# Optimization experiments

Hardware: AMD Instinct MI355X
Metric: run time of the kernel (lower is better)

Reference implementation:

```python
import jax, jax.numpy as jnp
import numpy as np

Z_DIM = 128
K = 64
RANK = 16
B = 65536


def setup_inputs() -> dict:
    key = jax.random.key(0)
    k1, k2, k3 = jax.random.split(key, 3)
    z = jax.random.normal(k1, (B, Z_DIM), dtype=jnp.float32)
    # nn.Linear(z_dim, K*rank): weight [K*rank, z_dim], bias [K*rank]
    bound = 1.0 / np.sqrt(Z_DIM)
    W = jax.random.uniform(k2, (K * RANK, Z_DIM), dtype=jnp.float32, minval=-bound, maxval=bound)
    b = jax.random.uniform(k3, (K * RANK,), dtype=jnp.float32, minval=-bound, maxval=bound)
    return {"z": z, "W": W, "b": b}


def reference(z, W, b):
    bsz = z.shape[0]
    # linear projection: [B, K*rank]
    w = z @ W.T + b
    w = w.reshape(bsz, K, RANK) + 1e-6
    # batched reduced QR on small K x rank matrices (fp32, like torch .float())
    q, _ = jnp.linalg.qr(w.astype(jnp.float32), mode="reduced")
    return q.astype(z.dtype)
```

## Files before the change

kernel.cpp:

```cpp
#include <hip/hip_runtime.h>

#define TOTAL_B 65536
#define NKR 1024
#define ZD 128

__global__ __launch_bounds__(256) void gemm_zwt(
    const float* __restrict__ z, const float* __restrict__ W,
    const float* __restrict__ bias, float* __restrict__ out)
{
    __shared__ float zs[32][132];
    __shared__ float ws[32][132];

    const int tid = threadIdx.x;
    const int tx = tid & 15;
    const int ty = tid >> 4;
    const int m0 = blockIdx.y * 128;
    const int n0 = blockIdx.x * 128;

    float acc[8][8];
    #pragma unroll
    for (int i = 0; i < 8; ++i)
        #pragma unroll
        for (int j = 0; j < 8; ++j) acc[i][j] = 0.f;

    const int kq = (tid & 7) * 4;
    const int mr = tid >> 3;

    const float* gz = z + (size_t)(m0 + mr) * ZD + kq;
    const float* gw = W + (size_t)(n0 + mr) * ZD + kq;

    float4 vz[4], vw[4];
    #pragma unroll
    for (int p = 0; p < 4; ++p) {
        vz[p] = *(const float4*)(gz + (size_t)p * 32 * ZD);
        vw[p] = *(const float4*)(gw + (size_t)p * 32 * ZD);
    }

    #pragma unroll
    for (int kc = 0; kc < ZD; kc += 32) {
        #pragma unroll
        for (int p = 0; p < 4; ++p) {
            int ml = mr + p * 32;
            zs[kq + 0][ml] = vz[p].x; zs[kq + 1][ml] = vz[p].y;
            zs[kq + 2][ml] = vz[p].z; zs[kq + 3][ml] = vz[p].w;
            ws[kq + 0][ml] = vw[p].x; ws[kq + 1][ml] = vw[p].y;
            ws[kq + 2][ml] = vw[p].z; ws[kq + 3][ml] = vw[p].w;
        }
        __syncthreads();

        if (kc + 32 < ZD) {
            #pragma unroll
            for (int p = 0; p < 4; ++p) {
                vz[p] = *(const float4*)(gz + (size_t)p * 32 * ZD + kc + 32);
                vw[p] = *(const float4*)(gw + (size_t)p * 32 * ZD + kc + 32);
            }
        }

        #pragma unroll 8
        for (int k = 0; k < 32; ++k) {
            float4 a0 = *(const float4*)&zs[k][ty * 4];
            float4 a1 = *(const float4*)&zs[k][64 + ty * 4];
            float4 c0 = *(const float4*)&ws[k][tx * 4];
            float4 c1 = *(const float4*)&ws[k][64 + tx * 4];
            float zr[8] = {a0.x, a0.y, a0.z, a0.w, a1.x, a1.y, a1.z, a1.w};
            float wr[8] = {c0.x, c0.y, c0.z, c0.w, c1.x, c1.y, c1.z, c1.w};
            #pragma unroll
            for (int i = 0; i < 8; ++i)
                #pragma unroll
                for (int j = 0; j < 8; ++j)
                    acc[i][j] = fmaf(zr[i], wr[j], acc[i][j]);
        }
        __syncthreads();
    }

    float bv0[4], bv1[4];
    #pragma unroll
    for (int j = 0; j < 4; ++j) {
        bv0[j] = bias[n0 + tx * 4 + j] + 1e-6f;
        bv1[j] = bias[n0 + 64 + tx * 4 + j] + 1e-6f;
    }

    #pragma unroll
    for (int i = 0; i < 8; ++i) {
        int row = (i < 4) ? (ty * 4 + i) : (64 + ty * 4 + i - 4);
        size_t base = (size_t)(m0 + row) * NKR + n0;
        float4 o0, o1;
        o0.x = acc[i][0] + bv0[0]; o0.y = acc[i][1] + bv0[1];
        o0.z = acc[i][2] + bv0[2]; o0.w = acc[i][3] + bv0[3];
        o1.x = acc[i][4] + bv1[0]; o1.y = acc[i][5] + bv1[1];
        o1.z = acc[i][6] + bv1[2]; o1.w = acc[i][7] + bv1[3];
        *(float4*)(out + base + tx * 4) = o0;
        *(float4*)(out + base + 64 + tx * 4) = o1;
    }
}

template <int CTRL>
__device__ __forceinline__ float dpp_add(float v) {
    int x = __builtin_amdgcn_update_dpp(0, __float_as_int(v), CTRL, 0xF, 0xF, false);
    return v + __int_as_float(x);
}

__device__ __forceinline__ float rsum16(float v) {
    v = dpp_add<0x128>(v);
    v = dpp_add<0x124>(v);
    v = dpp_add<0x122>(v);
    v = dpp_add<0x121>(v);
    return v;
}

__global__ __launch_bounds__(256) void qr_batched(float* __restrict__ buf)
{
    const int tid = threadIdx.x;
    const int lq = tid & 15;
    const int item = (blockIdx.x * 256 + tid) >> 4;

    float* p = buf + (size_t)item * NKR + lq * 16;

    float a[16][4];
    #pragma unroll
    for (int i = 0; i < 4; ++i) {
        #pragma unroll
        for (int cc = 0; cc < 16; cc += 4) {
            float4 v = *(const float4*)(p + i * 256 + cc);
            a[cc + 0][i] = v.x; a[cc + 1][i] = v.y;
            a[cc + 2][i] = v.z; a[cc + 3][i] = v.w;
        }
    }

    float tau[16];

    #pragma unroll
    for (int j = 0; j < 16; ++j) {
        float x0 = a[j][0], x1 = a[j][1], x2 = a[j][2], x3 = a[j][3];
        float x0m = (lq > j) ? x0 : 0.f;
        float pp = fmaf(x0m, x0m, fmaf(x1, x1, fmaf(x2, x2, x3 * x3)));
        float xn2   = rsum16(pp);
        float alpha = rsum16((lq == j) ? x0 : 0.f);

        float rr   = __builtin_amdgcn_sqrtf(fmaf(alpha, alpha, xn2));
        float beta = (alpha >= 0.f) ? -rr : rr;
        float dba  = beta - alpha;
        float tj   = dba * __builtin_amdgcn_rcpf(beta);
        float sc   = -__builtin_amdgcn_rcpf(dba);
        if (xn2 == 0.f) { tj = 0.f; sc = 0.f; }
        tau[j] = tj;

        float v0 = (lq == j) ? 1.f : ((lq > j) ? x0 * sc : 0.f);
        float v1 = x1 * sc, v2 = x2 * sc, v3 = x3 * sc;
        a[j][0] = v0; a[j][1] = v1; a[j][2] = v2; a[j][3] = v3;

        #pragma unroll
        for (int c = j + 1; c < 16; ++c) {
            float d = rsum16(fmaf(v0, a[c][0],
                        fmaf(v1, a[c][1],
                        fmaf(v2, a[c][2], v3 * a[c][3]))));
            float t = -tj * d;
            a[c][0] = fmaf(t, v0, a[c][0]);
            a[c][1] = fmaf(t, v1, a[c][1]);
            a[c][2] = fmaf(t, v2, a[c][2]);
            a[c][3] = fmaf(t, v3, a[c][3]);
        }
    }

    #pragma unroll
    for (int j = 15; j >= 0; --j) {
        float tj = tau[j];
        float v0 = a[j][0], v1 = a[j][1], v2 = a[j][2], v3 = a[j][3];
        #pragma unroll
        for (int c = j + 1; c < 16; ++c) {
            float d = rsum16(fmaf(v0, a[c][0],
                        fmaf(v1, a[c][1],
                        fmaf(v2, a[c][2], v3 * a[c][3]))));
            float t = -tj * d;
            a[c][0] = fmaf(t, v0, a[c][0]);
            a[c][1] = fmaf(t, v1, a[c][1]);
            a[c][2] = fmaf(t, v2, a[c][2]);
            a[c][3] = fmaf(t, v3, a[c][3]);
        }
        float nt = -tj;
        a[j][0] = fmaf(nt, v0, (lq == j) ? 1.f : 0.f);
        a[j][1] = nt * v1;
        a[j][2] = nt * v2;
        a[j][3] = nt * v3;
    }

    #pragma unroll
    for (int i = 0; i < 4; ++i) {
        #pragma unroll
        for (int cc = 0; cc < 16; cc += 4) {
            float4 vv = {a[cc + 0][i], a[cc + 1][i], a[cc + 2][i], a[cc + 3][i]};
            *(float4*)(p + i * 256 + cc) = vv;
        }
    }
}

extern "C" void kernel_launch(void* const* d_in, const int* in_sizes, int n_in,
                              void* d_out, int out_size, void* d_ws, size_t ws_size,
                              hipStream_t stream) {
    const float* z = (const float*)d_in[0];
    const float* W = (const float*)d_in[1];
    const float* b = (const float*)d_in[2];
    float* out = (float*)d_out;

    dim3 ggrid(NKR / 128, TOTAL_B / 128);
    hipLaunchKernelGGL(gemm_zwt, ggrid, dim3(256), 0, stream, z, W, b, out);
    hipLaunchKernelGGL(qr_batched, dim3(TOTAL_B / 16), dim3(256), 0, stream, out);
}
```

Measured before the change: 605.1 us.

## Store GEMM tiles row-major in LDS and use strided thread-to-output mapping

The GEMM kernel now keeps z and W tiles in shared memory in their natural row-major layout, padded to 36, instead of transposing them on store. The inner loop reads float4 along K and does four FMAs per pair. The thread-to-output mapping becomes strided (ty+16i, tx+16j), so outputs are written as scalar stores, coalesced across threads, instead of float4 stores. The grid is swapped so blockIdx.x walks the batch dimension, and the register prefetch of the next K chunk is dropped, which removes overlap between global loads and compute.

Result: slower. 625.5 us (+3.4%).

```diff
diff --git a/kernel.cpp b/kernel.cpp
--- a/kernel.cpp
+++ b/kernel.cpp
@@ -8,14 +8,14 @@
     const float* __restrict__ z, const float* __restrict__ W,
     const float* __restrict__ bias, float* __restrict__ out)
 {
-    __shared__ float zs[32][132];
-    __shared__ float ws[32][132];
+    __shared__ float zs[128][36];
+    __shared__ float ws[128][36];
 
     const int tid = threadIdx.x;
     const int tx = tid & 15;
     const int ty = tid >> 4;
-    const int m0 = blockIdx.y * 128;
-    const int n0 = blockIdx.x * 128;
+    const int m0 = blockIdx.x * 128;
+    const int n0 = blockIdx.y * 128;
 
     float acc[8][8];
     #pragma unroll
@@ -29,68 +29,50 @@
     const float* gz = z + (size_t)(m0 + mr) * ZD + kq;
     const float* gw = W + (size_t)(n0 + mr) * ZD + kq;
 
-    float4 vz[4], vw[4];
-    #pragma unroll
-    for (int p = 0; p < 4; ++p) {
-        vz[p] = *(const float4*)(gz + (size_t)p * 32 * ZD);
-        vw[p] = *(const float4*)(gw + (size_t)p * 32 * ZD);
-    }
-
-    #pragma unroll
     for (int kc = 0; kc < ZD; kc += 32) {
         #pragma unroll
         for (int p = 0; p < 4; ++p) {
-            int ml = mr + p * 32;
-            zs[kq + 0][ml] = vz[p].x; zs[kq + 1][ml] = vz[p].y;
-            zs[kq + 2][ml] = vz[p].z; zs[kq + 3][ml] = vz[p].w;
-            ws[kq + 0][ml] = vw[p].x; ws[kq + 1][ml] = vw[p].y;
-            ws[kq + 2][ml] = vw[p].z; ws[kq + 3][ml] = vw[p].w;
+            int row = mr + p * 32;
+            float4 vz = *(const float4*)(gz + (size_t)p * 32 * ZD + kc);
+            float4 vw = *(const float4*)(gw + (size_t)p * 32 * ZD + kc);
+            *(float4*)&zs[row][kq] = vz;
+            *(float4*)&ws[row][kq] = vw;
         }
         __syncthreads();
 
-        if (kc + 32 < ZD) {
-            #pragma unroll
-            for (int p = 0; p < 4; ++p) {
-                vz[p] = *(const float4*)(gz + (size_t)p * 32 * ZD + kc + 32);
-                vw[p] = *(const float4*)(gw + (size_t)p * 32 * ZD + kc + 32);
-            }
-        }
-
-        #pragma unroll 8
-        for (int k = 0; k < 32; ++k) {
-            float4 a0 = *(const float4*)&zs[k][ty * 4];
-            float4 a1 = *(const float4*)&zs[k][64 + ty * 4];
-            float4 c0 = *(const float4*)&ws[k][tx * 4];
-            float4 c1 = *(const float4*)&ws[k][64 + tx * 4];
-            float zr[8] = {a0.x, a0.y, a0.z, a0.w, a1.x, a1.y, a1.z, a1.w};
-            float wr[8] = {c0.x, c0.y, c0.z, c0.w, c1.x, c1.y, c1.z, c1.w};
+        #pragma unroll
+        for (int k4 = 0; k4 < 8; ++k4) {
+            float4 za[8];
             #pragma unroll
             for (int i = 0; i < 8; ++i)
+                za[i] = *(const float4*)&zs[ty + 16 * i][k4 * 4];
+            #pragma unroll
+            for (int j = 0; j < 8; ++j) {
+                float4 wa = *(const float4*)&ws[tx + 16 * j][k4 * 4];
                 #pragma unroll
-                for (int j = 0; j < 8; ++j)
-                    acc[i][j] = fmaf(zr[i], wr[j], acc[i][j]);
+                for (int i = 0; i < 8; ++i) {
+                    float s = acc[i][j];
+                    s = fmaf(za[i].x, wa.x, s);
+                    s = fmaf(za[i].y, wa.y, s);
+                    s = fmaf(za[i].z, wa.z, s);
+                    s = fmaf(za[i].w, wa.w, s);
+                    acc[i][j] = s;
+                }
+            }
         }
         __syncthreads();
     }
 
-    float bv0[4], bv1[4];
+    float bv[8];
     #pragma unroll
-    for (int j = 0; j < 4; ++j) {
-        bv0[j] = bias[n0 + tx * 4 + j] + 1e-6f;
-        bv1[j] = bias[n0 + 64 + tx * 4 + j] + 1e-6f;
-    }
+    for (int j = 0; j < 8; ++j) bv[j] = bias[n0 + tx + 16 * j] + 1e-6f;
 
     #pragma unroll
     for (int i = 0; i < 8; ++i) {
-        int row = (i < 4) ? (ty * 4 + i) : (64 + ty * 4 + i - 4);
-        size_t base = (size_t)(m0 + row) * NKR + n0;
-        float4 o0, o1;
-        o0.x = acc[i][0] + bv0[0]; o0.y = acc[i][1] + bv0[1];
-        o0.z = acc[i][2] + bv0[2]; o0.w = acc[i][3] + bv0[3];
-        o1.x = acc[i][4] + bv1[0]; o1.y = acc[i][5] + bv1[1];
-        o1.z = acc[i][6] + bv1[2]; o1.w = acc[i][7] + bv1[3];
-        *(float4*)(out + base + tx * 4) = o0;
-        *(float4*)(out + base + 64 + tx * 4) = o1;
+        size_t base = (size_t)(m0 + ty + 16 * i) * NKR + n0;
+        #pragma unroll
+        for (int j = 0; j < 8; ++j)
+            out[base + tx + 16 * j] = acc[i][j] + bv[j];
     }
 }
 
@@ -202,7 +184,7 @@
     const float* b = (const float*)d_in[2];
     float* out = (float*)d_out;
 
-    dim3 ggrid(NKR / 128, TOTAL_B / 128);
+    dim3 ggrid(TOTAL_B / 128, NKR / 128);
     hipLaunchKernelGGL(gemm_zwt, ggrid, dim3(256), 0, stream, z, W, b, out);
     hipLaunchKernelGGL(qr_batched, dim3(TOTAL_B / 16), dim3(256), 0, stream, out);
 }
```
